# Kernel optimization log

Hardware: AMD Instinct MI355X
Metric: run time of the kernel (lower is better)

## Reference

```python
import jax, jax.numpy as jnp
import numpy as np

EXPERT_ID = 3
NUM_EXPERTS = 8
FULL_DIM = 4096
EXPERT_DIM = 1024
SLICE = FULL_DIM // NUM_EXPERTS          # 512
S0 = EXPERT_ID * SLICE
S1 = S0 + SLICE
FP_MIN = EXPERT_ID / NUM_EXPERTS         # 0.375
FP_MAX = (EXPERT_ID + 1) / NUM_EXPERTS   # 0.5
GATE_HID = SLICE // 4                    # 128


def _xavier(key, shape):
    fan_out, fan_in = shape
    lim = float(np.sqrt(6.0 / (fan_in + fan_out)))
    return jax.random.uniform(key, shape, minval=-lim, maxval=lim, dtype=jnp.float32)


def setup_inputs() -> dict:
    key = jax.random.key(0)
    ks = jax.random.split(key, 9)
    B, P = 4, 4096
    tokens = jax.random.normal(ks[0], (B, P, FULL_DIM), dtype=jnp.float32)
    fingerprints = jax.random.uniform(ks[1], (P,), dtype=jnp.float32)
    # learned params (torch nn.Linear stores weight as [out, in])
    gate_w1 = _xavier(ks[2], (GATE_HID, SLICE))
    gate_b1 = jnp.zeros((GATE_HID,), dtype=jnp.float32)
    gate_w2 = _xavier(ks[3], (1, GATE_HID))
    gate_b2 = jnp.zeros((1,), dtype=jnp.float32)
    wq = _xavier(ks[4], (EXPERT_DIM, SLICE))
    wk = _xavier(ks[5], (EXPERT_DIM, SLICE))
    wv = _xavier(ks[6], (EXPERT_DIM, SLICE))
    penta = jax.random.normal(ks[7], (5, EXPERT_DIM), dtype=jnp.float32) * 0.02
    penta = penta / jnp.linalg.norm(penta, axis=-1, keepdims=True)  # _init_weights normalizes
    alpha = jnp.asarray(1.0, dtype=jnp.float32)
    return {
        'tokens': tokens, 'fingerprints': fingerprints, 'alpha': alpha,
        'gate_w1': gate_w1, 'gate_b1': gate_b1, 'gate_w2': gate_w2, 'gate_b2': gate_b2,
        'wq': wq, 'wk': wk, 'wv': wv, 'pentachoron': penta,
    }


def reference(tokens, fingerprints, alpha, gate_w1, gate_b1, gate_w2, gate_b2,
              wq, wk, wv, pentachoron):
    # expert 3 is not the last expert -> strict upper bound
    mask = (fingerprints >= FP_MIN) & (fingerprints < FP_MAX)        # [P] bool
    # gather selected patches, then slice this expert's feature band
    my_features = tokens[..., S0:S1][:, mask]                        # [B, p, SLICE]
    # gating MLP: Linear -> GELU(exact) -> Linear -> Sigmoid
    h = jax.nn.gelu(my_features @ gate_w1.T + gate_b1, approximate=False)
    alpha_gate = jax.nn.sigmoid(h @ gate_w2.T + gate_b2)             # [B, p, 1]
    alpha_weight = jax.nn.sigmoid(alpha)
    my_features = my_features * (alpha_gate * alpha_weight + (1.0 - alpha_weight))
    Q = my_features @ wq.T                                           # [B, p, D]
    K = my_features @ wk.T
    V = my_features @ wv.T
    # per-vertex affinities, vectorized over the 5 pentachoron vertices
    dirs = pentachoron / jnp.linalg.norm(pentachoron, axis=-1, keepdims=True)
    K_aff = jnp.einsum('bpd,vd->vbp', K, dirs)                       # [5, B, p]
    Q_aff = jnp.einsum('bpd,vd->vbp', Q, dirs)
    return (Q, K, V, K_aff, Q_aff, mask)
```

## Files before the change

kernel.cpp:

```cpp
#include <hip/hip_runtime.h>
#include <hip/hip_bf16.h>

#define FULL_DIM 4096
#define EXPERT_DIM 1024
#define SLICE 512
#define S0 (3*SLICE)
#define GATE_HID 128
#define P_TOK 4096
#define BATCH 4
#define NCONV 192
#define NCW 32

typedef __bf16 bf16;
typedef __bf16 bf16x4 __attribute__((ext_vector_type(4)));
typedef __bf16 bf16x8 __attribute__((ext_vector_type(8)));
typedef float f32x4 __attribute__((ext_vector_type(4)));

__device__ inline void gl_lds16(const void* g, void* l) {
    __builtin_amdgcn_global_load_lds((const __attribute__((address_space(1))) void*)g,
                                     (__attribute__((address_space(3))) void*)l, 16, 0, 0);
}

__device__ inline bf16x8 cvt8(const float* src) {
    float4 a = *(const float4*)(src);
    float4 b = *(const float4*)(src + 4);
    bf16x8 w = { (bf16)a.x, (bf16)a.y, (bf16)a.z, (bf16)a.w,
                 (bf16)b.x, (bf16)b.y, (bf16)b.z, (bf16)b.w };
    return w;
}

__launch_bounds__(256)
__global__ void k_front(const float* __restrict__ tokens, const float* __restrict__ fp,
                        const float* __restrict__ alpha,
                        const float* __restrict__ gw1, const float* __restrict__ gb1,
                        const float* __restrict__ gw2, const float* __restrict__ gb2,
                        const float* __restrict__ wq, const float* __restrict__ wk,
                        const float* __restrict__ wv, const float* __restrict__ penta,
                        bf16* __restrict__ wqkvb, float* __restrict__ cwp,
                        float* __restrict__ mask_out, bf16* __restrict__ Fs,
                        int p, int M, int ngate) {
    __shared__ bf16 F[32][520];
    __shared__ int trow[32];
    __shared__ float scl[32];
    __shared__ float part[32][4];
    __shared__ int sOffs[256];
    __shared__ unsigned short sBits[256];
    __shared__ int wsum[4];
    __shared__ float sd[5][32];
    __shared__ float red[5][4];
    const int bid = blockIdx.x, t = threadIdx.x;
    const int wave = t >> 6, lane = t & 63;

    if (bid < ngate) {
        const int fr = lane & 15, fq = lane >> 4;
        const int m0 = bid * 32;
        {
            int base = t * 16;
            unsigned bits = 0;
            int cnt = 0;
#pragma unroll
            for (int i = 0; i < 16; i++) {
                float v = fp[base + i];
                bool m = (v >= 0.375f) && (v < 0.5f);
                bits |= ((unsigned)m) << i;
                cnt += (int)m;
            }
            int incl = cnt;
#pragma unroll
            for (int d = 1; d < 64; d <<= 1) {
                int n = __shfl_up(incl, d);
                if (lane >= d) incl += n;
            }
            if (lane == 63) wsum[wave] = incl;
            __syncthreads();
            int wbase = 0;
            for (int w = 0; w < 4; w++) if (w < wave) wbase += wsum[w];
            sOffs[t] = wbase + incl - cnt;
            sBits[t] = (unsigned short)bits;
        }
        __syncthreads();
        if (t < 32) {
            int m = m0 + t;
            int r = -1;
            if (m < M) {
                int b = m / p, j = m - b * p;
                int lo = 0, hi = 255;
                while (lo < hi) { int mid = (lo + hi + 1) >> 1; if (sOffs[mid] <= j) lo = mid; else hi = mid - 1; }
                int jj = j - sOffs[lo];
                unsigned bt = sBits[lo];
                int pos = 0;
#pragma unroll
                for (int bit = 0; bit < 16; bit++) {
                    if ((bt >> bit) & 1) { if (jj == 0) { pos = bit; break; } jj--; }
                }
                r = b * P_TOK + lo * 16 + pos;
            }
            trow[t] = r;
        }
        __syncthreads();
#pragma unroll
        for (int it = 0; it < 16; it++) {
            int r = it * 2 + (t >> 7);
            int c4 = (t & 127) * 4;
            int tr = trow[r];
            float4 v = {0.f, 0.f, 0.f, 0.f};
            if (tr >= 0) v = *(const float4*)(tokens + (size_t)tr * FULL_DIM + S0 + c4);
            bf16x4 b = { (bf16)v.x, (bf16)v.y, (bf16)v.z, (bf16)v.w };
            *(bf16x4*)(&F[r][c4]) = b;
        }
        __syncthreads();
        f32x4 acc[2][2];
#pragma unroll
        for (int i = 0; i < 2; i++)
#pragma unroll
            for (int j = 0; j < 2; j++) acc[i][j] = (f32x4){0.f, 0.f, 0.f, 0.f};
        const int n0 = wave * 32 + fr;
#pragma unroll
        for (int k0 = 0; k0 < 512; k0 += 64) {
#pragma unroll
            for (int ks = 0; ks < 2; ks++) {
                const int ko = k0 + ks * 32 + fq * 8;
                bf16x8 b0 = cvt8(gw1 + (size_t)n0 * 512 + ko);
                bf16x8 b1 = cvt8(gw1 + (size_t)(n0 + 16) * 512 + ko);
                bf16x8 a0 = *(const bf16x8*)(&F[fr][ko]);
                bf16x8 a1 = *(const bf16x8*)(&F[16 + fr][ko]);
                acc[0][0] = __builtin_amdgcn_mfma_f32_16x16x32_bf16(a0, b0, acc[0][0], 0, 0, 0);
                acc[0][1] = __builtin_amdgcn_mfma_f32_16x16x32_bf16(a0, b1, acc[0][1], 0, 0, 0);
                acc[1][0] = __builtin_amdgcn_mfma_f32_16x16x32_bf16(a1, b0, acc[1][0], 0, 0, 0);
                acc[1][1] = __builtin_amdgcn_mfma_f32_16x16x32_bf16(a1, b1, acc[1][1], 0, 0, 0);
            }
        }
        {
            float s[2][4];
#pragma unroll
            for (int mi = 0; mi < 2; mi++)
#pragma unroll
                for (int r = 0; r < 4; r++) s[mi][r] = 0.f;
#pragma unroll
            for (int ni = 0; ni < 2; ni++) {
                int col = wave * 32 + ni * 16 + fr;
                float bias = gb1[col], g2 = gw2[col];
#pragma unroll
                for (int mi = 0; mi < 2; mi++)
#pragma unroll
                    for (int r = 0; r < 4; r++) {
                        float v = acc[mi][ni][r] + bias;
                        float h = 0.5f * v * (1.0f + erff(v * 0.70710678118f));
                        s[mi][r] += h * g2;
                    }
            }
#pragma unroll
            for (int mi = 0; mi < 2; mi++)
#pragma unroll
                for (int r = 0; r < 4; r++) {
                    float v = s[mi][r];
                    v += __shfl_xor(v, 1); v += __shfl_xor(v, 2);
                    v += __shfl_xor(v, 4); v += __shfl_xor(v, 8);
                    s[mi][r] = v;
                }
            if (fr == 0) {
#pragma unroll
                for (int mi = 0; mi < 2; mi++)
#pragma unroll
                    for (int r = 0; r < 4; r++)
                        part[mi * 16 + fq * 4 + r][wave] = s[mi][r];
            }
        }
        __syncthreads();
        if (t < 32) {
            float ssum = part[t][0] + part[t][1] + part[t][2] + part[t][3];
            float aw = 1.0f / (1.0f + expf(-alpha[0]));
            float gt = 1.0f / (1.0f + expf(-(ssum + gb2[0])));
            scl[t] = gt * aw + (1.0f - aw);
        }
        __syncthreads();
#pragma unroll
        for (int it = 0; it < 16; it++) {
            int r = it * 2 + (t >> 7);
            int c4 = (t & 127) * 4;
            bf16x4 b = *(const bf16x4*)(&F[r][c4]);
            float sc = scl[r];
            bf16x4 o = { (bf16)((float)b[0] * sc), (bf16)((float)b[1] * sc),
                         (bf16)((float)b[2] * sc), (bf16)((float)b[3] * sc) };
            *(bf16x4*)(Fs + (size_t)(m0 + r) * 512 + c4) = o;
        }
        return;
    }
    if (bid == ngate) {
        int base = t * 16;
#pragma unroll
        for (int i = 0; i < 16; i++) {
            float v = fp[base + i];
            mask_out[base + i] = ((v >= 0.375f) && (v < 0.5f)) ? 1.0f : 0.0f;
        }
        return;
    }
    if (bid <= ngate + NCW) {
        const int cb = bid - (ngate + 1);
        const int d0 = cb * 32;
#pragma unroll
        for (int v = 0; v < 5; v++) {
            float s = 0.f;
#pragma unroll
            for (int i = 0; i < 4; i++) { float x = penta[v * 1024 + t + i * 256]; s += x * x; }
            for (int d = 32; d; d >>= 1) s += __shfl_xor(s, d);
            if (lane == 0) red[v][wave] = s;
        }
        __syncthreads();
        for (int e = t; e < 5 * 32; e += 256) {
            int v = e >> 5, dd = e & 31;
            float inv = rsqrtf(red[v][0] + red[v][1] + red[v][2] + red[v][3]);
            sd[v][dd] = penta[v * 1024 + d0 + dd] * inv;
        }
        __syncthreads();
#pragma unroll
        for (int pass = 0; pass < 2; pass++) {
            int col = pass * 256 + t;
            float aK[5] = {0, 0, 0, 0, 0}, aQ[5] = {0, 0, 0, 0, 0};
            for (int d = 0; d < 32; d += 4) {
#pragma unroll
                for (int uu = 0; uu < 4; uu++) {
                    float kv = wk[(size_t)(d0 + d + uu) * 512 + col];
                    float qv = wq[(size_t)(d0 + d + uu) * 512 + col];
#pragma unroll
                    for (int v = 0; v < 5; v++) {
                        float dv = sd[v][d + uu];
                        aK[v] += dv * kv;
                        aQ[v] += dv * qv;
                    }
                }
            }
#pragma unroll
            for (int v = 0; v < 5; v++) {
                cwp[((size_t)v * NCW + cb) * 512 + col] = aK[v];
                cwp[((size_t)(5 + v) * NCW + cb) * 512 + col] = aQ[v];
            }
        }
        return;
    }
    {
        int ci = bid - (ngate + 1 + NCW);
        int base = ci * 8192 + t * 4;
        const float* src = (base < 524288) ? wq : (base < 2 * 524288 ? wk : wv);
        const int arr = base & 524287;
#pragma unroll
        for (int q = 0; q < 8; q++) {
            int i = arr + q * 1024;
            float4 v = *(const float4*)(src + i);
            bf16x4 b = { (bf16)v.x, (bf16)v.y, (bf16)v.z, (bf16)v.w };
            *(bf16x4*)(wqkvb + (base < 524288 ? 0 : (base < 2 * 524288 ? 524288 : 2 * 524288)) + i) = b;
        }
    }
}

__launch_bounds__(512)
__global__ void k_qkv(const bf16* __restrict__ A, const bf16* __restrict__ W,
                      const float* __restrict__ cwp, float* __restrict__ out,
                      float* __restrict__ aff, int M) {
    __shared__ bf16 As[2][256 * 64];
    __shared__ bf16 Bs[2][128 * 64];
    const int t = threadIdx.x, wave = t >> 6, lane = t & 63;
    const int fr = lane & 15, fq = lane >> 4;

    if (blockIdx.y == 24) {
        bf16* cwt = (bf16*)As;
        for (int e = t; e < 16 * 512; e += 512) {
            int v = e >> 9, c = e & 511;
            float s = 0.f;
            if (v < 10) {
#pragma unroll
                for (int cb = 0; cb < NCW; cb++)
                    s += cwp[((size_t)v * NCW + cb) * 512 + c];
            }
            int byte = v * 1024 + ((((c >> 3) ^ (v & 7)) << 4)) + (c & 7) * 2;
            *(bf16*)((char*)cwt + byte) = (bf16)s;
        }
        __syncthreads();
        const int m0w = blockIdx.x * 256 + wave * 32;
        f32x4 acc0 = (f32x4){0.f, 0.f, 0.f, 0.f};
        f32x4 acc1 = (f32x4){0.f, 0.f, 0.f, 0.f};
        for (int k0 = 0; k0 < 512; k0 += 32) {
            int chunk = (k0 >> 3) + fq;
            bf16x8 b = *(const bf16x8*)((char*)cwt + fr * 1024 + ((chunk ^ (fr & 7)) << 4));
            bf16x8 a0 = *(const bf16x8*)(A + (size_t)(m0w + fr) * 512 + k0 + fq * 8);
            bf16x8 a1 = *(const bf16x8*)(A + (size_t)(m0w + 16 + fr) * 512 + k0 + fq * 8);
            acc0 = __builtin_amdgcn_mfma_f32_16x16x32_bf16(a0, b, acc0, 0, 0, 0);
            acc1 = __builtin_amdgcn_mfma_f32_16x16x32_bf16(a1, b, acc1, 0, 0, 0);
        }
        if (fr < 10) {
#pragma unroll
            for (int r = 0; r < 4; r++) {
                int m = m0w + fq * 4 + r;
                if (m < M) aff[(size_t)fr * M + m] = acc0[r];
                m += 16;
                if (m < M) aff[(size_t)fr * M + m] = acc1[r];
            }
        }
        return;
    }

    const int m0 = blockIdx.x * 256, n0 = blockIdx.y * 128;
    const int wr = wave >> 1, wc = wave & 1;

    f32x4 acc[4][4];
#pragma unroll
    for (int i = 0; i < 4; i++)
#pragma unroll
        for (int j = 0; j < 4; j++) acc[i][j] = (f32x4){0.f, 0.f, 0.f, 0.f};

    const int lr = lane >> 3;
    const int js = (lane & 7) ^ lr;
    const bf16* gaL = A + (size_t)(m0 + wave * 32 + lr) * 512 + js * 8;
    const bf16* gbL = W + (size_t)(n0 + wave * 16 + lr) * 512 + js * 8;
    const int xr = fr & 7;

#define STAGE(buf, ko)                                                \
    gl_lds16(gaL + (ko),            &As[buf][(wave * 4 + 0) * 512]);  \
    gl_lds16(gaL + (ko) +  8 * 512, &As[buf][(wave * 4 + 1) * 512]);  \
    gl_lds16(gaL + (ko) + 16 * 512, &As[buf][(wave * 4 + 2) * 512]);  \
    gl_lds16(gaL + (ko) + 24 * 512, &As[buf][(wave * 4 + 3) * 512]);  \
    gl_lds16(gbL + (ko),            &Bs[buf][(wave * 2 + 0) * 512]);  \
    gl_lds16(gbL + (ko) +  8 * 512, &Bs[buf][(wave * 2 + 1) * 512]);

#define COMPUTE(buf)                                                                      \
    _Pragma("unroll")                                                                     \
    for (int ks = 0; ks < 2; ks++) {                                                      \
        const int co = ((ks * 4 + fq) ^ xr) * 8;                                          \
        bf16x8 af[4], bw[4];                                                              \
        _Pragma("unroll")                                                                 \
        for (int mi = 0; mi < 4; mi++)                                                    \
            af[mi] = *(const bf16x8*)(&As[buf][(wr * 64 + mi * 16 + fr) * 64 + co]);      \
        _Pragma("unroll")                                                                 \
        for (int ni = 0; ni < 4; ni++)                                                    \
            bw[ni] = *(const bf16x8*)(&Bs[buf][(wc * 64 + ni * 16 + fr) * 64 + co]);      \
        _Pragma("unroll")                                                                 \
        for (int mi = 0; mi < 4; mi++)                                                    \
            _Pragma("unroll")                                                             \
            for (int ni = 0; ni < 4; ni++)                                                \
                acc[mi][ni] = __builtin_amdgcn_mfma_f32_16x16x32_bf16(af[mi], bw[ni], acc[mi][ni], 0, 0, 0); \
    }

    STAGE(0, 0);
    int cur = 0;
#pragma unroll 1
    for (int kt = 0; kt < 8; kt++) {
        if (kt < 7) {
            STAGE(cur ^ 1, (kt + 1) * 64);
            asm volatile("s_waitcnt vmcnt(6)" ::: "memory");
        } else {
            asm volatile("s_waitcnt vmcnt(0)" ::: "memory");
        }
        __builtin_amdgcn_s_barrier();
        COMPUTE(cur);
        __builtin_amdgcn_s_barrier();
        cur ^= 1;
    }
#undef STAGE
#undef COMPUTE

    const int z = blockIdx.y >> 3;
    const int nb = (blockIdx.y & 7) * 128;
    float* obase = out + (size_t)z * M * EXPERT_DIM;
#pragma unroll
    for (int mi = 0; mi < 4; mi++)
#pragma unroll
        for (int ni = 0; ni < 4; ni++) {
            int col = nb + wc * 64 + ni * 16 + fr;
#pragma unroll
            for (int r = 0; r < 4; r++) {
                int row = m0 + wr * 64 + mi * 16 + fq * 4 + r;
                if (row < M) obase[(size_t)row * EXPERT_DIM + col] = acc[mi][ni][r];
            }
        }
}

extern "C" void kernel_launch(void* const* d_in, const int* in_sizes, int n_in,
                              void* d_out, int out_size, void* d_ws, size_t ws_size,
                              hipStream_t stream) {
    const float* tokens = (const float*)d_in[0];
    const float* fps    = (const float*)d_in[1];
    const float* alpha  = (const float*)d_in[2];
    const float* gw1    = (const float*)d_in[3];
    const float* gb1    = (const float*)d_in[4];
    const float* gw2    = (const float*)d_in[5];
    const float* gb2    = (const float*)d_in[6];
    const float* wq     = (const float*)d_in[7];
    const float* wk     = (const float*)d_in[8];
    const float* wv     = (const float*)d_in[9];
    const float* penta  = (const float*)d_in[10];
    float* out = (float*)d_out;

    int p = (out_size - P_TOK) / (3 * BATCH * EXPERT_DIM + 2 * 5 * BATCH);
    if (p <= 0) return;
    int M = BATCH * p;
    int Mpad = (M + 255) & ~255;
    int ngate = Mpad / 32;

    char* ws = (char*)d_ws;
    size_t off = 0;
    bf16*  wqkvb = (bf16*)(ws + off);  off += (size_t)3 * EXPERT_DIM * SLICE * 2;
    float* cwp   = (float*)(ws + off); off += (size_t)NCW * 10 * 512 * 4;
    bf16*  Fs    = (bf16*)(ws + off);  off += (size_t)Mpad * SLICE * 2;
    (void)ws_size;

    float* aff_out  = out + (size_t)3 * M * EXPERT_DIM;
    float* mask_out = aff_out + (size_t)10 * M;

    k_front<<<ngate + 1 + NCW + NCONV, 256, 0, stream>>>(
        tokens, fps, alpha, gw1, gb1, gw2, gb2, wq, wk, wv, penta,
        wqkvb, cwp, mask_out, Fs, p, M, ngate);
    k_qkv<<<dim3(Mpad / 256, 25), 512, 0, stream>>>(Fs, wqkvb, cwp, out, aff_out, M);
}
```

Baseline: 50.94 us.

## Merge front and GEMM kernels into one persistent launch with a grid barrier

Folds the gating/prep kernel and the QKV GEMM kernel into a single launch. A global atomic-counter barrier separates the prep phase from the GEMM phase, which removes one kernel launch and the gap between the two kernels. The GEMM tile shrinks to 128x128 with 256 threads, 32-wide K steps and a shared union LDS buffer. The weight bf16 conversion is also reassigned to 24 blocks, one per GEMM column tile. A software grid barrier needs every block to be co-resident and adds a memset, and it can deadlock if the grid exceeds device occupancy.

After: 88.18 us. +73.1%, slower.

```diff
diff --git a/kernel.cpp b/kernel.cpp
--- a/kernel.cpp
+++ b/kernel.cpp
@@ -5,10 +5,8 @@
 #define EXPERT_DIM 1024
 #define SLICE 512
 #define S0 (3*SLICE)
-#define GATE_HID 128
 #define P_TOK 4096
 #define BATCH 4
-#define NCONV 192
 #define NCW 32
 
 typedef __bf16 bf16;
@@ -29,17 +27,18 @@
     return w;
 }
 
-__launch_bounds__(256)
-__global__ void k_front(const float* __restrict__ tokens, const float* __restrict__ fp,
-                        const float* __restrict__ alpha,
-                        const float* __restrict__ gw1, const float* __restrict__ gb1,
-                        const float* __restrict__ gw2, const float* __restrict__ gb2,
-                        const float* __restrict__ wq, const float* __restrict__ wk,
-                        const float* __restrict__ wv, const float* __restrict__ penta,
-                        bf16* __restrict__ wqkvb, float* __restrict__ cwp,
-                        float* __restrict__ mask_out, bf16* __restrict__ Fs,
-                        int p, int M, int ngate) {
-    __shared__ bf16 F[32][520];
+__launch_bounds__(256, 2)
+__global__ void k_all(const float* __restrict__ tokens, const float* __restrict__ fp,
+                      const float* __restrict__ alpha,
+                      const float* __restrict__ gw1, const float* __restrict__ gb1,
+                      const float* __restrict__ gw2, const float* __restrict__ gb2,
+                      const float* __restrict__ wq, const float* __restrict__ wk,
+                      const float* __restrict__ wv, const float* __restrict__ penta,
+                      bf16* __restrict__ wqkvb, float* __restrict__ cwp,
+                      float* __restrict__ mask_out, bf16* __restrict__ Fs,
+                      float* __restrict__ out, float* __restrict__ aff,
+                      unsigned* bar, int p, int M, int Mpad, int nblk) {
+    __shared__ __align__(16) char ubuf[33280];
     __shared__ int trow[32];
     __shared__ float scl[32];
     __shared__ float part[32][4];
@@ -48,11 +47,18 @@
     __shared__ int wsum[4];
     __shared__ float sd[5][32];
     __shared__ float red[5][4];
+
     const int bid = blockIdx.x, t = threadIdx.x;
     const int wave = t >> 6, lane = t & 63;
+    const int fr = lane & 15, fq = lane >> 4;
+    const int ngate = Mpad / 32;
+    const int nx = Mpad / 128;
+    const int ngemm = nx * 24;
+    const int cwbase = ngate + 2;
+    const int cvbase = (ngate + 41) & ~7;
 
     if (bid < ngate) {
-        const int fr = lane & 15, fq = lane >> 4;
+        bf16 (*F)[520] = (bf16(*)[520])ubuf;
         const int m0 = bid * 32;
         {
             int base = t * 16;
@@ -184,19 +190,15 @@
                          (bf16)((float)b[2] * sc), (bf16)((float)b[3] * sc) };
             *(bf16x4*)(Fs + (size_t)(m0 + r) * 512 + c4) = o;
         }
-        return;
-    }
-    if (bid == ngate) {
+    } else if (bid == ngate) {
         int base = t * 16;
 #pragma unroll
         for (int i = 0; i < 16; i++) {
             float v = fp[base + i];
             mask_out[base + i] = ((v >= 0.375f) && (v < 0.5f)) ? 1.0f : 0.0f;
         }
-        return;
-    }
-    if (bid <= ngate + NCW) {
-        const int cb = bid - (ngate + 1);
+    } else if (bid >= cwbase && bid < cwbase + NCW) {
+        const int cb = bid - cwbase;
         const int d0 = cb * 32;
 #pragma unroll
         for (int v = 0; v < 5; v++) {
@@ -236,35 +238,108 @@
                 cwp[((size_t)(5 + v) * NCW + cb) * 512 + col] = aQ[v];
             }
         }
-        return;
-    }
-    {
-        int ci = bid - (ngate + 1 + NCW);
-        int base = ci * 8192 + t * 4;
-        const float* src = (base < 524288) ? wq : (base < 2 * 524288 ? wk : wv);
-        const int arr = base & 524287;
-#pragma unroll
-        for (int q = 0; q < 8; q++) {
-            int i = arr + q * 1024;
+    } else if (bid >= cvbase && bid < cvbase + 24) {
+        int y = bid - cvbase;
+        const float* src = (y < 8) ? wq : (y < 16 ? wk : wv);
+        src += (size_t)(y & 7) * 128 * 512;
+        bf16* dst = wqkvb + (size_t)y * 128 * 512;
+#pragma unroll 4
+        for (int it = 0; it < 64; it++) {
+            int i = it * 1024 + t * 4;
             float4 v = *(const float4*)(src + i);
             bf16x4 b = { (bf16)v.x, (bf16)v.y, (bf16)v.z, (bf16)v.w };
-            *(bf16x4*)(wqkvb + (base < 524288 ? 0 : (base < 2 * 524288 ? 524288 : 2 * 524288)) + i) = b;
+            *(bf16x4*)(dst + i) = b;
         }
     }
-}
-
-__launch_bounds__(512)
-__global__ void k_qkv(const bf16* __restrict__ A, const bf16* __restrict__ W,
-                      const float* __restrict__ cwp, float* __restrict__ out,
-                      float* __restrict__ aff, int M) {
-    __shared__ bf16 As[2][256 * 64];
-    __shared__ bf16 Bs[2][128 * 64];
-    const int t = threadIdx.x, wave = t >> 6, lane = t & 63;
-    const int fr = lane & 15, fq = lane >> 4;
-
-    if (blockIdx.y == 24) {
-        bf16* cwt = (bf16*)As;
-        for (int e = t; e < 16 * 512; e += 512) {
+
+    __syncthreads();
+    if (t == 0) {
+        __threadfence();
+        atomicAdd(bar, 1u);
+        while (__hip_atomic_load(bar, __ATOMIC_RELAXED, __HIP_MEMORY_SCOPE_AGENT) < (unsigned)nblk)
+            __builtin_amdgcn_s_sleep(8);
+        __threadfence();
+    }
+    __syncthreads();
+
+    if (bid < ngemm) {
+        const int y = bid % 24, x = bid / 24;
+        const int m0 = x * 128, n0g = y * 128;
+        const int wr = wave >> 1, wc = wave & 1;
+        bf16* As = (bf16*)ubuf;
+        bf16* Bs = (bf16*)(ubuf + 16384);
+
+        f32x4 acc[4][4];
+#pragma unroll
+        for (int i = 0; i < 4; i++)
+#pragma unroll
+            for (int j = 0; j < 4; j++) acc[i][j] = (f32x4){0.f, 0.f, 0.f, 0.f};
+
+        const int lr4 = lane >> 2;
+        const int js = (lane & 3) ^ (lr4 & 3);
+        const bf16* gaL = Fs    + (size_t)(m0  + wave * 32 + lr4) * 512 + js * 8;
+        const bf16* gbL = wqkvb + (size_t)(n0g + wave * 32 + lr4) * 512 + js * 8;
+        const int xr3 = fr & 3;
+
+#define STAGE(buf, ko)                                                      \
+        gl_lds16(gaL + (ko),            As + (buf) * 4096 + (wave * 32) * 32);        \
+        gl_lds16(gaL + (ko) + 16 * 512, As + (buf) * 4096 + (wave * 32 + 16) * 32);   \
+        gl_lds16(gbL + (ko),            Bs + (buf) * 4096 + (wave * 32) * 32);        \
+        gl_lds16(gbL + (ko) + 16 * 512, Bs + (buf) * 4096 + (wave * 32 + 16) * 32);
+
+#define COMPUTE(buf)                                                                     \
+        {                                                                                \
+            const int co = (fq ^ xr3) * 8;                                               \
+            bf16x8 af[4], bw[4];                                                         \
+            _Pragma("unroll")                                                            \
+            for (int mi = 0; mi < 4; mi++)                                               \
+                af[mi] = *(const bf16x8*)(As + (buf) * 4096 + (wr * 64 + mi * 16 + fr) * 32 + co); \
+            _Pragma("unroll")                                                            \
+            for (int ni = 0; ni < 4; ni++)                                               \
+                bw[ni] = *(const bf16x8*)(Bs + (buf) * 4096 + (wc * 64 + ni * 16 + fr) * 32 + co); \
+            _Pragma("unroll")                                                            \
+            for (int mi = 0; mi < 4; mi++)                                               \
+                _Pragma("unroll")                                                        \
+                for (int ni = 0; ni < 4; ni++)                                           \
+                    acc[mi][ni] = __builtin_amdgcn_mfma_f32_16x16x32_bf16(af[mi], bw[ni], acc[mi][ni], 0, 0, 0); \
+        }
+
+        STAGE(0, 0);
+        int cur = 0;
+#pragma unroll 1
+        for (int kt = 0; kt < 16; kt++) {
+            if (kt < 15) {
+                STAGE(cur ^ 1, (kt + 1) * 32);
+                asm volatile("s_waitcnt vmcnt(4)" ::: "memory");
+            } else {
+                asm volatile("s_waitcnt vmcnt(0)" ::: "memory");
+            }
+            __builtin_amdgcn_s_barrier();
+            COMPUTE(cur);
+            __builtin_amdgcn_s_barrier();
+            cur ^= 1;
+        }
+#undef STAGE
+#undef COMPUTE
+
+        const int z = y >> 3;
+        const int nb = (y & 7) * 128;
+        float* obase = out + (size_t)z * M * EXPERT_DIM;
+#pragma unroll
+        for (int mi = 0; mi < 4; mi++)
+#pragma unroll
+            for (int ni = 0; ni < 4; ni++) {
+                int col = nb + wc * 64 + ni * 16 + fr;
+#pragma unroll
+                for (int r = 0; r < 4; r++) {
+                    int row = m0 + wr * 64 + mi * 16 + fq * 4 + r;
+                    if (row < M) obase[(size_t)row * EXPERT_DIM + col] = acc[mi][ni][r];
+                }
+            }
+    } else if (bid < ngemm + nx) {
+        const int ax = bid - ngemm;
+        bf16* cwt = (bf16*)ubuf;
+        for (int e = t; e < 16 * 512; e += 256) {
             int v = e >> 9, c = e & 511;
             float s = 0.f;
             if (v < 10) {
@@ -276,14 +351,14 @@
             *(bf16*)((char*)cwt + byte) = (bf16)s;
         }
         __syncthreads();
-        const int m0w = blockIdx.x * 256 + wave * 32;
+        const int m0w = ax * 128 + wave * 32;
         f32x4 acc0 = (f32x4){0.f, 0.f, 0.f, 0.f};
         f32x4 acc1 = (f32x4){0.f, 0.f, 0.f, 0.f};
         for (int k0 = 0; k0 < 512; k0 += 32) {
             int chunk = (k0 >> 3) + fq;
             bf16x8 b = *(const bf16x8*)((char*)cwt + fr * 1024 + ((chunk ^ (fr & 7)) << 4));
-            bf16x8 a0 = *(const bf16x8*)(A + (size_t)(m0w + fr) * 512 + k0 + fq * 8);
-            bf16x8 a1 = *(const bf16x8*)(A + (size_t)(m0w + 16 + fr) * 512 + k0 + fq * 8);
+            bf16x8 a0 = *(const bf16x8*)(Fs + (size_t)(m0w + fr) * 512 + k0 + fq * 8);
+            bf16x8 a1 = *(const bf16x8*)(Fs + (size_t)(m0w + 16 + fr) * 512 + k0 + fq * 8);
             acc0 = __builtin_amdgcn_mfma_f32_16x16x32_bf16(a0, b, acc0, 0, 0, 0);
             acc1 = __builtin_amdgcn_mfma_f32_16x16x32_bf16(a1, b, acc1, 0, 0, 0);
         }
@@ -296,82 +371,7 @@
                 if (m < M) aff[(size_t)fr * M + m] = acc1[r];
             }
         }
-        return;
     }
-
-    const int m0 = blockIdx.x * 256, n0 = blockIdx.y * 128;
-    const int wr = wave >> 1, wc = wave & 1;
-
-    f32x4 acc[4][4];
-#pragma unroll
-    for (int i = 0; i < 4; i++)
-#pragma unroll
-        for (int j = 0; j < 4; j++) acc[i][j] = (f32x4){0.f, 0.f, 0.f, 0.f};
-
-    const int lr = lane >> 3;
-    const int js = (lane & 7) ^ lr;
-    const bf16* gaL = A + (size_t)(m0 + wave * 32 + lr) * 512 + js * 8;
-    const bf16* gbL = W + (size_t)(n0 + wave * 16 + lr) * 512 + js * 8;
-    const int xr = fr & 7;
-
-#define STAGE(buf, ko)                                                \
-    gl_lds16(gaL + (ko),            &As[buf][(wave * 4 + 0) * 512]);  \
-    gl_lds16(gaL + (ko) +  8 * 512, &As[buf][(wave * 4 + 1) * 512]);  \
-    gl_lds16(gaL + (ko) + 16 * 512, &As[buf][(wave * 4 + 2) * 512]);  \
-    gl_lds16(gaL + (ko) + 24 * 512, &As[buf][(wave * 4 + 3) * 512]);  \
-    gl_lds16(gbL + (ko),            &Bs[buf][(wave * 2 + 0) * 512]);  \
-    gl_lds16(gbL + (ko) +  8 * 512, &Bs[buf][(wave * 2 + 1) * 512]);
-
-#define COMPUTE(buf)                                                                      \
-    _Pragma("unroll")                                                                     \
-    for (int ks = 0; ks < 2; ks++) {                                                      \
-        const int co = ((ks * 4 + fq) ^ xr) * 8;                                          \
-        bf16x8 af[4], bw[4];                                                              \
-        _Pragma("unroll")                                                                 \
-        for (int mi = 0; mi < 4; mi++)                                                    \
-            af[mi] = *(const bf16x8*)(&As[buf][(wr * 64 + mi * 16 + fr) * 64 + co]);      \
-        _Pragma("unroll")                                                                 \
-        for (int ni = 0; ni < 4; ni++)                                                    \
-            bw[ni] = *(const bf16x8*)(&Bs[buf][(wc * 64 + ni * 16 + fr) * 64 + co]);      \
-        _Pragma("unroll")                                                                 \
-        for (int mi = 0; mi < 4; mi++)                                                    \
-            _Pragma("unroll")                                                             \
-            for (int ni = 0; ni < 4; ni++)                                                \
-                acc[mi][ni] = __builtin_amdgcn_mfma_f32_16x16x32_bf16(af[mi], bw[ni], acc[mi][ni], 0, 0, 0); \
-    }
-
-    STAGE(0, 0);
-    int cur = 0;
-#pragma unroll 1
-    for (int kt = 0; kt < 8; kt++) {
-        if (kt < 7) {
-            STAGE(cur ^ 1, (kt + 1) * 64);
-            asm volatile("s_waitcnt vmcnt(6)" ::: "memory");
-        } else {
-            asm volatile("s_waitcnt vmcnt(0)" ::: "memory");
-        }
-        __builtin_amdgcn_s_barrier();
-        COMPUTE(cur);
-        __builtin_amdgcn_s_barrier();
-        cur ^= 1;
-    }
-#undef STAGE
-#undef COMPUTE
-
-    const int z = blockIdx.y >> 3;
-    const int nb = (blockIdx.y & 7) * 128;
-    float* obase = out + (size_t)z * M * EXPERT_DIM;
-#pragma unroll
-    for (int mi = 0; mi < 4; mi++)
-#pragma unroll
-        for (int ni = 0; ni < 4; ni++) {
-            int col = nb + wc * 64 + ni * 16 + fr;
-#pragma unroll
-            for (int r = 0; r < 4; r++) {
-                int row = m0 + wr * 64 + mi * 16 + fq * 4 + r;
-                if (row < M) obase[(size_t)row * EXPERT_DIM + col] = acc[mi][ni][r];
-            }
-        }
 }
 
 extern "C" void kernel_launch(void* const* d_in, const int* in_sizes, int n_in,
@@ -393,11 +393,11 @@
     int p = (out_size - P_TOK) / (3 * BATCH * EXPERT_DIM + 2 * 5 * BATCH);
     if (p <= 0) return;
     int M = BATCH * p;
-    int Mpad = (M + 255) & ~255;
-    int ngate = Mpad / 32;
+    int Mpad = (M + 127) & ~127;
 
     char* ws = (char*)d_ws;
     size_t off = 0;
+    unsigned* bar  = (unsigned*)(ws + off); off += 256;
     bf16*  wqkvb = (bf16*)(ws + off);  off += (size_t)3 * EXPERT_DIM * SLICE * 2;
     float* cwp   = (float*)(ws + off); off += (size_t)NCW * 10 * 512 * 4;
     bf16*  Fs    = (bf16*)(ws + off);  off += (size_t)Mpad * SLICE * 2;
@@ -406,8 +406,15 @@
     float* aff_out  = out + (size_t)3 * M * EXPERT_DIM;
     float* mask_out = aff_out + (size_t)10 * M;
 
-    k_front<<<ngate + 1 + NCW + NCONV, 256, 0, stream>>>(
-        tokens, fps, alpha, gw1, gb1, gw2, gb2, wq, wk, wv, penta,
-        wqkvb, cwp, mask_out, Fs, p, M, ngate);
-    k_qkv<<<dim3(Mpad / 256, 25), 512, 0, stream>>>(Fs, wqkvb, cwp, out, aff_out, M);
+    int ngate = Mpad / 32;
+    int nx = Mpad / 128;
+    int ngemm = nx * 24;
+    int cvbase = (ngate + 41) & ~7;
+    int nblk = ngemm + nx;
+    if (cvbase + 24 > nblk) nblk = cvbase + 24;
+
+    hipMemsetAsync(bar, 0, 256, stream);
+    k_all<<<nblk, 256, 0, stream>>>(tokens, fps, alpha, gw1, gb1, gw2, gb2,
+                                    wq, wk, wv, penta, wqkvb, cwp, mask_out, Fs,
+                                    out, aff_out, bar, p, M, Mpad, nblk);
 }
```

## Shrink QKV GEMM tile to 128x128x32 with 1D grid and new swizzle

Applied to the files above, without the earlier changes.

Changes the QKV GEMM block tile from 256x128 with K-step 64 (512 threads) to 128x128 with K-step 32 (256 threads). The launch becomes a 1D grid in which the M-tile index varies slowest, and the affinity blocks are appended at the end. The LDS swizzle is reworked for 32-wide rows. The aim is more blocks for better CU occupancy and tail balance at this modest M, and smaller LDS use per block. In exchange there are twice as many K iterations and barriers, and each A tile is reused across fewer N columns.

Result: slower. 57.57 us (+13.0%).

```diff
diff --git a/kernel.cpp b/kernel.cpp
--- a/kernel.cpp
+++ b/kernel.cpp
@@ -253,18 +253,21 @@
     }
 }
 
-__launch_bounds__(512)
+__launch_bounds__(256)
 __global__ void k_qkv(const bf16* __restrict__ A, const bf16* __restrict__ W,
                       const float* __restrict__ cwp, float* __restrict__ out,
-                      float* __restrict__ aff, int M) {
-    __shared__ bf16 As[2][256 * 64];
-    __shared__ bf16 Bs[2][128 * 64];
+                      float* __restrict__ aff, int M, int nx) {
+    __shared__ bf16 As[2][128 * 32];
+    __shared__ bf16 Bs[2][128 * 32];
     const int t = threadIdx.x, wave = t >> 6, lane = t & 63;
     const int fr = lane & 15, fq = lane >> 4;
-
-    if (blockIdx.y == 24) {
+    const int bid = blockIdx.x;
+    const int ngemm = nx * 24;
+
+    if (bid >= ngemm) {
+        const int ax = bid - ngemm;
         bf16* cwt = (bf16*)As;
-        for (int e = t; e < 16 * 512; e += 512) {
+        for (int e = t; e < 16 * 512; e += 256) {
             int v = e >> 9, c = e & 511;
             float s = 0.f;
             if (v < 10) {
@@ -276,7 +279,7 @@
             *(bf16*)((char*)cwt + byte) = (bf16)s;
         }
         __syncthreads();
-        const int m0w = blockIdx.x * 256 + wave * 32;
+        const int m0w = ax * 128 + wave * 32;
         f32x4 acc0 = (f32x4){0.f, 0.f, 0.f, 0.f};
         f32x4 acc1 = (f32x4){0.f, 0.f, 0.f, 0.f};
         for (int k0 = 0; k0 < 512; k0 += 32) {
@@ -299,7 +302,8 @@
         return;
     }
 
-    const int m0 = blockIdx.x * 256, n0 = blockIdx.y * 128;
+    const int y = bid % 24, x = bid / 24;
+    const int m0 = x * 128, n0 = y * 128;
     const int wr = wave >> 1, wc = wave & 1;
 
     f32x4 acc[4][4];
@@ -308,31 +312,29 @@
 #pragma unroll
         for (int j = 0; j < 4; j++) acc[i][j] = (f32x4){0.f, 0.f, 0.f, 0.f};
 
-    const int lr = lane >> 3;
-    const int js = (lane & 7) ^ lr;
+    const int lr = lane >> 2;
+    const int key = (lr ^ (lr >> 2)) & 3;
+    const int js = (lane & 3) ^ key;
     const bf16* gaL = A + (size_t)(m0 + wave * 32 + lr) * 512 + js * 8;
-    const bf16* gbL = W + (size_t)(n0 + wave * 16 + lr) * 512 + js * 8;
-    const int xr = fr & 7;
+    const bf16* gbL = W + (size_t)(n0 + wave * 32 + lr) * 512 + js * 8;
+    const int kr = (fr ^ (fr >> 2)) & 3;
 
 #define STAGE(buf, ko)                                                \
-    gl_lds16(gaL + (ko),            &As[buf][(wave * 4 + 0) * 512]);  \
-    gl_lds16(gaL + (ko) +  8 * 512, &As[buf][(wave * 4 + 1) * 512]);  \
-    gl_lds16(gaL + (ko) + 16 * 512, &As[buf][(wave * 4 + 2) * 512]);  \
-    gl_lds16(gaL + (ko) + 24 * 512, &As[buf][(wave * 4 + 3) * 512]);  \
+    gl_lds16(gaL + (ko),            &As[buf][(wave * 2 + 0) * 512]);  \
+    gl_lds16(gaL + (ko) + 16 * 512, &As[buf][(wave * 2 + 1) * 512]);  \
     gl_lds16(gbL + (ko),            &Bs[buf][(wave * 2 + 0) * 512]);  \
-    gl_lds16(gbL + (ko) +  8 * 512, &Bs[buf][(wave * 2 + 1) * 512]);
+    gl_lds16(gbL + (ko) + 16 * 512, &Bs[buf][(wave * 2 + 1) * 512]);
 
 #define COMPUTE(buf)                                                                      \
-    _Pragma("unroll")                                                                     \
-    for (int ks = 0; ks < 2; ks++) {                                                      \
-        const int co = ((ks * 4 + fq) ^ xr) * 8;                                          \
+    {                                                                                     \
+        const int co = ((fq ^ kr)) * 8;                                                   \
         bf16x8 af[4], bw[4];                                                              \
         _Pragma("unroll")                                                                 \
         for (int mi = 0; mi < 4; mi++)                                                    \
-            af[mi] = *(const bf16x8*)(&As[buf][(wr * 64 + mi * 16 + fr) * 64 + co]);      \
+            af[mi] = *(const bf16x8*)(&As[buf][(wr * 64 + mi * 16 + fr) * 32 + co]);      \
         _Pragma("unroll")                                                                 \
         for (int ni = 0; ni < 4; ni++)                                                    \
-            bw[ni] = *(const bf16x8*)(&Bs[buf][(wc * 64 + ni * 16 + fr) * 64 + co]);      \
+            bw[ni] = *(const bf16x8*)(&Bs[buf][(wc * 64 + ni * 16 + fr) * 32 + co]);      \
         _Pragma("unroll")                                                                 \
         for (int mi = 0; mi < 4; mi++)                                                    \
             _Pragma("unroll")                                                             \
@@ -343,10 +345,10 @@
     STAGE(0, 0);
     int cur = 0;
 #pragma unroll 1
-    for (int kt = 0; kt < 8; kt++) {
-        if (kt < 7) {
-            STAGE(cur ^ 1, (kt + 1) * 64);
-            asm volatile("s_waitcnt vmcnt(6)" ::: "memory");
+    for (int kt = 0; kt < 16; kt++) {
+        if (kt < 15) {
+            STAGE(cur ^ 1, (kt + 1) * 32);
+            asm volatile("s_waitcnt vmcnt(4)" ::: "memory");
         } else {
             asm volatile("s_waitcnt vmcnt(0)" ::: "memory");
         }
@@ -358,8 +360,8 @@
 #undef STAGE
 #undef COMPUTE
 
-    const int z = blockIdx.y >> 3;
-    const int nb = (blockIdx.y & 7) * 128;
+    const int z = y >> 3;
+    const int nb = (y & 7) * 128;
     float* obase = out + (size_t)z * M * EXPERT_DIM;
 #pragma unroll
     for (int mi = 0; mi < 4; mi++)
@@ -393,8 +395,9 @@
     int p = (out_size - P_TOK) / (3 * BATCH * EXPERT_DIM + 2 * 5 * BATCH);
     if (p <= 0) return;
     int M = BATCH * p;
-    int Mpad = (M + 255) & ~255;
+    int Mpad = (M + 127) & ~127;
     int ngate = Mpad / 32;
+    int nx = Mpad / 128;
 
     char* ws = (char*)d_ws;
     size_t off = 0;
@@ -409,5 +412,5 @@
     k_front<<<ngate + 1 + NCW + NCONV, 256, 0, stream>>>(
         tokens, fps, alpha, gw1, gb1, gw2, gb2, wq, wk, wv, penta,
         wqkvb, cwp, mask_out, Fs, p, M, ngate);
-    k_qkv<<<dim3(Mpad / 256, 25), 512, 0, stream>>>(Fs, wqkvb, cwp, out, aff_out, M);
+    k_qkv<<<nx * 24 + nx, 256, 0, stream>>>(Fs, wqkvb, cwp, out, aff_out, M, nx);
 }
```
